# Optimization experiments

Measured on AMD Instinct MI355X. Metric: run time of the kernel, lower is better.

The kernel has to match this reference:

```python
import jax, jax.numpy as jnp
import numpy as np

B, L, D, H, FFN = 4, 1024, 1024, 16, 4096
DPH = D // H
EPS = 1e-5

def layer_norm(x, g, b):
    mu = jnp.mean(x, axis=-1, keepdims=True)
    var = jnp.mean(jnp.square(x - mu), axis=-1, keepdims=True)
    return (x - mu) * jax.lax.rsqrt(var + EPS) * g + b

def setup_inputs() -> dict:
    key = jax.random.key(0)
    ks = jax.random.split(key, 12)
    s = 0.02
    return {
        "inputs": jax.random.normal(ks[0], (B, L, D), dtype=jnp.float32),
        "Wq": jax.random.normal(ks[1], (D, D), dtype=jnp.float32) * s,
        "bq": jnp.zeros((D,), jnp.float32),
        "Wk": jax.random.normal(ks[2], (D, D), dtype=jnp.float32) * s,
        "bk": jnp.zeros((D,), jnp.float32),
        "Wv": jax.random.normal(ks[3], (D, D), dtype=jnp.float32) * s,
        "bv": jnp.zeros((D,), jnp.float32),
        "Wo": jax.random.normal(ks[4], (D, D), dtype=jnp.float32) * s,
        "bo": jnp.zeros((D,), jnp.float32),
        "ln1_g": jnp.ones((D,), jnp.float32),
        "ln1_b": jnp.zeros((D,), jnp.float32),
        "W1": jax.random.normal(ks[5], (D, FFN), dtype=jnp.float32) * s,  # conv1d k=1 == linear
        "b1": jnp.zeros((FFN,), jnp.float32),
        "W2": jax.random.normal(ks[6], (FFN, D), dtype=jnp.float32) * s,
        "b2": jnp.zeros((D,), jnp.float32),
        "ln2_g": jnp.ones((D,), jnp.float32),
        "ln2_b": jnp.zeros((D,), jnp.float32),
    }

def reference(inputs, Wq, bq, Wk, bk, Wv, bv, Wo, bo, ln1_g, ln1_b,
              W1, b1, W2, b2, ln2_g, ln2_b):
    residual = inputs
    # QKV projections, then the original's raw view(B*H, L, DPH) split (NOT a transpose split)
    q = (inputs @ Wq + bq).reshape(B * H, L, DPH)
    k = (inputs @ Wk + bk).reshape(B * H, L, DPH)
    v = (inputs @ Wv + bv).reshape(B * H, L, DPH)
    scale = DPH ** -0.5
    scores = jnp.einsum('bqd,bkd->bqk', q, k) * scale  # [B*H, L, L]
    attention = jax.nn.softmax(scores, axis=-1)
    context = jnp.einsum('bqk,bkd->bqd', attention, v).reshape(B, L, D)
    out = context @ Wo + bo
    out = layer_norm(residual + out, ln1_g, ln1_b)
    # Positionwise FFN: two 1x1 conv1d == two linears with relu
    ffn = jax.nn.relu(out @ W1 + b1) @ W2 + b2
    out = layer_norm(out + ffn, ln2_g, ln2_b)
    return out, attention
```

## Files before the change

kernel.cpp:

```cpp
#include <hip/hip_runtime.h>
#include <hip/hip_bf16.h>
#include <stdint.h>


using bf16_t  = __hip_bfloat16;
using short8  = __attribute__((ext_vector_type(8))) short;
using short4v = __attribute__((ext_vector_type(4))) short;
using f32x4   = __attribute__((ext_vector_type(4))) float;

#define DEV static __device__ __forceinline__

DEV short bfbits(float f) {
  bf16_t h = __float2bfloat16(f);
  union { bf16_t h; short s; } u; u.h = h; return u.s;
}

DEV void gload_lds16(const bf16_t* g, bf16_t* lds) {
  __builtin_amdgcn_global_load_lds(
      (const __attribute__((address_space(1))) void*)g,
      (__attribute__((address_space(3))) void*)lds, 16, 0, 0);
}

__global__ __launch_bounds__(256) void k_f32_to_bf16(const float* __restrict__ in,
                                                     bf16_t* __restrict__ out) {
  size_t i = ((size_t)blockIdx.x * 256 + threadIdx.x) * 4;
  f32x4 x = *(const f32x4*)(in + i);
  short4v o;
  o[0] = bfbits(x[0]); o[1] = bfbits(x[1]); o[2] = bfbits(x[2]); o[3] = bfbits(x[3]);
  *(short4v*)((short*)out + i) = o;
}

__global__ __launch_bounds__(256) void k_transpose_f32_bf16(const float* __restrict__ in,
                                                            bf16_t* __restrict__ out,
                                                            int R, int C) {
  __shared__ float tile[32][33];
  int tx = threadIdx.x & 31, ty = threadIdx.x >> 5;
  int r0 = blockIdx.y * 32, c0 = blockIdx.x * 32;
  #pragma unroll
  for (int i = 0; i < 4; ++i)
    tile[ty + i * 8][tx] = in[(size_t)(r0 + ty + i * 8) * C + c0 + tx];
  __syncthreads();
  #pragma unroll
  for (int i = 0; i < 4; ++i)
    out[(size_t)(c0 + ty + i * 8) * R + r0 + tx] = __float2bfloat16(tile[tx][ty + i * 8]);
}

__global__ __launch_bounds__(256) void k_transpose4_f32_bf16(
    const float* __restrict__ w0, const float* __restrict__ w1,
    const float* __restrict__ w2, const float* __restrict__ w3,
    bf16_t* __restrict__ o0, bf16_t* __restrict__ o1,
    bf16_t* __restrict__ o2, bf16_t* __restrict__ o3) {
  __shared__ float tile[32][33];
  const int zz = blockIdx.z;
  const float* in = zz == 0 ? w0 : zz == 1 ? w1 : zz == 2 ? w2 : w3;
  bf16_t* out = zz == 0 ? o0 : zz == 1 ? o1 : zz == 2 ? o2 : o3;
  int tx = threadIdx.x & 31, ty = threadIdx.x >> 5;
  int r0 = blockIdx.y * 32, c0 = blockIdx.x * 32;
  #pragma unroll
  for (int i = 0; i < 4; ++i)
    tile[ty + i * 8][tx] = in[(size_t)(r0 + ty + i * 8) * 1024 + c0 + tx];
  __syncthreads();
  #pragma unroll
  for (int i = 0; i < 4; ++i)
    out[(size_t)(c0 + ty + i * 8) * 1024 + r0 + tx] = __float2bfloat16(tile[tx][ty + i * 8]);
}

__global__ __launch_bounds__(256) void k_transpose_bf16_b(const bf16_t* __restrict__ in,
                                                          bf16_t* __restrict__ out,
                                                          int R, int C, long sIn, long sOut) {
  __shared__ bf16_t tile[32][33];
  const bf16_t* inz = in + (size_t)blockIdx.z * sIn;
  bf16_t* outz = out + (size_t)blockIdx.z * sOut;
  int tx = threadIdx.x & 31, ty = threadIdx.x >> 5;
  int r0 = blockIdx.y * 32, c0 = blockIdx.x * 32;
  #pragma unroll
  for (int i = 0; i < 4; ++i)
    tile[ty + i * 8][tx] = inz[(size_t)(r0 + ty + i * 8) * C + c0 + tx];
  __syncthreads();
  #pragma unroll
  for (int i = 0; i < 4; ++i)
    outz[(size_t)(c0 + ty + i * 8) * R + r0 + tx] = tile[tx][ty + i * 8];
}

template<int BM, int BN, bool ALPHA, bool BIAS, bool RELU, bool RESID,
         bool OUTF, bool OUTB, bool QKV3>
__global__ __launch_bounds__(256)
void k_gemm_bt(const bf16_t* __restrict__ A, const bf16_t* __restrict__ Bt,
               float* __restrict__ Cf, bf16_t* __restrict__ Cb,
               const float* __restrict__ bias, const float* __restrict__ bias2,
               const float* __restrict__ bias3, const float* __restrict__ resid,
               int Kdim, int lda, int ldb, int ldc, float alpha) {
  constexpr int BK = 32;
  constexpr int WTM = BM / 2, WTN = BN / 2;
  constexpr int MI = WTM / 16, NI = WTN / 16;
  __shared__ __align__(16) bf16_t sA[BM * BK];
  __shared__ __align__(16) bf16_t sB[BN * BK];

  const int tid = threadIdx.x;
  const int lane = tid & 63;
  const int wv = tid >> 6;
  const int wm = wv & 1, wn = wv >> 1;

  const int gx = gridDim.x;
  const int total = gx * gridDim.y;
  const int lin = blockIdx.y * gx + blockIdx.x;
  const int swz = (lin & 7) * (total >> 3) + (lin >> 3);
  const size_t m0 = (size_t)(swz / gx) * BM;
  const size_t n0 = (size_t)(swz % gx) * BN;

  f32x4 acc[MI][NI] = {};

  const int rr = lane >> 2, cc = (lane & 3) * 8;
  const bf16_t* Arow = A + (m0 + rr) * (size_t)lda + cc;
  const bf16_t* Brow = Bt + (n0 + rr) * (size_t)ldb + cc;

  const int fm = wm * WTM + (lane & 15);
  const int fn = wn * WTN + (lane & 15);
  const int fk = (lane >> 4) * 8;

  for (int k0 = 0; k0 < Kdim; k0 += BK) {
    #pragma unroll
    for (int j = 0; j < BM / 64; ++j) {
      int c = j * 4 + wv;
      gload_lds16(Arow + (size_t)c * 16 * lda + k0, sA + c * 512);
    }
    #pragma unroll
    for (int j = 0; j < BN / 64; ++j) {
      int c = j * 4 + wv;
      gload_lds16(Brow + (size_t)c * 16 * ldb + k0, sB + c * 512);
    }
    __syncthreads();

    short8 av[MI], bvv[NI];
    #pragma unroll
    for (int mi = 0; mi < MI; ++mi) av[mi] = *(const short8*)(sA + (fm + mi * 16) * BK + fk);
    #pragma unroll
    for (int ni = 0; ni < NI; ++ni) bvv[ni] = *(const short8*)(sB + (fn + ni * 16) * BK + fk);
    #pragma unroll
    for (int mi = 0; mi < MI; ++mi)
      #pragma unroll
      for (int ni = 0; ni < NI; ++ni)
        acc[mi][ni] = __builtin_amdgcn_mfma_f32_16x16x32_bf16(av[mi], bvv[ni],
                                                              acc[mi][ni], 0, 0, 0);
    __syncthreads();
  }

  const int tz = QKV3 ? (int)(n0 >> 10) : 0;
  const float* bp = BIAS ? (QKV3 ? (tz == 0 ? bias : (tz == 1 ? bias2 : bias3))
                                 : bias) : nullptr;
  bf16_t* cb = QKV3 ? (Cb + (size_t)tz * 4194304) : Cb;
  const float qscale = (QKV3 && tz == 0) ? 0.125f : 1.0f;
  const int col0 = (int)n0 + wn * WTN + (lane & 15);
  const int row0 = (int)m0 + wm * WTM + ((lane >> 4) << 2);
  #pragma unroll
  for (int ni = 0; ni < NI; ++ni) {
    const int col = col0 + ni * 16;
    const int colw = QKV3 ? (col & 1023) : col;
    const float bval = BIAS ? bp[colw] : 0.0f;
    #pragma unroll
    for (int mi = 0; mi < MI; ++mi) {
      #pragma unroll
      for (int r = 0; r < 4; ++r) {
        int row = row0 + mi * 16 + r;
        float v = acc[mi][ni][r];
        if (ALPHA) v *= alpha;
        v += bval;
        if (QKV3) v *= qscale;
        size_t off = (size_t)row * ldc + colw;
        if (RESID) v += resid[off];
        if (RELU) v = fmaxf(v, 0.0f);
        if (OUTF) Cf[off] = v;
        if (OUTB) cb[off] = __float2bfloat16(v);
      }
    }
  }
}

__global__ __launch_bounds__(256) void k_flash_attn(const bf16_t* __restrict__ Qb,
                                                    const bf16_t* __restrict__ Kb,
                                                    const bf16_t* __restrict__ Vt,
                                                    float* __restrict__ attn,
                                                    bf16_t* __restrict__ ctx) {
  constexpr int LP = 72;
  __shared__ __align__(16) bf16_t sQ[128][LP];
  __shared__ __align__(16) bf16_t sK[2][64][LP];
  __shared__ __align__(16) bf16_t sV[2][64][LP];
  __shared__ __align__(16) bf16_t sP[128][LP];

  const int tid = threadIdx.x;
  const int lane = tid & 63;
  const int wv = tid >> 6;
  const int z = blockIdx.y;
  const int m0 = blockIdx.x * 128;

  const bf16_t* Qz = Qb + (size_t)z * 65536;
  const bf16_t* Kz = Kb + (size_t)z * 65536;
  const bf16_t* Vz = Vt + (size_t)z * 65536;
  float* az = attn + (size_t)z * 1048576;
  bf16_t* cz = ctx + (size_t)z * 65536;

  const int sr = tid >> 3, sc = (tid & 7) * 8;

  #pragma unroll
  for (int j = 0; j < 4; ++j)
    *(short8*)(&sQ[j * 32 + sr][sc]) =
        *(const short8*)(Qz + (size_t)(m0 + j * 32 + sr) * 64 + sc);
  __syncthreads();

  const int fr = lane & 15;
  const int fk = (lane >> 4) * 8;
  const int crow = (lane >> 4) << 2;

  short8 qf[2][2];
  #pragma unroll
  for (int mi = 0; mi < 2; ++mi)
    #pragma unroll
    for (int ks = 0; ks < 2; ++ks)
      qf[mi][ks] = *(const short8*)(&sQ[wv * 32 + mi * 16 + fr][ks * 32 + fk]);

  float m_run[2][4], s_run[2][4];
  #pragma unroll
  for (int mi = 0; mi < 2; ++mi)
    #pragma unroll
    for (int r = 0; r < 4; ++r) { m_run[mi][r] = -1e30f; s_run[mi][r] = 0.0f; }

  short8 kreg[2], vreg[2];

  #pragma unroll
  for (int j = 0; j < 2; ++j)
    kreg[j] = *(const short8*)(Kz + (size_t)(j * 32 + sr) * 64 + sc);
  #pragma unroll
  for (int j = 0; j < 2; ++j)
    *(short8*)(&sK[0][j * 32 + sr][sc]) = kreg[j];
  #pragma unroll
  for (int j = 0; j < 2; ++j)
    kreg[j] = *(const short8*)(Kz + (size_t)(64 + j * 32 + sr) * 64 + sc);
  __syncthreads();

  for (int c = 0; c < 16; ++c) {
    const int cur = c & 1;
    if (c + 1 < 16) {
      #pragma unroll
      for (int j = 0; j < 2; ++j)
        *(short8*)(&sK[cur ^ 1][j * 32 + sr][sc]) = kreg[j];
    }
    if (c + 2 < 16) {
      #pragma unroll
      for (int j = 0; j < 2; ++j)
        kreg[j] = *(const short8*)(Kz + (size_t)((c + 2) * 64 + j * 32 + sr) * 64 + sc);
    }
    f32x4 acc[2][4] = {};
    __builtin_amdgcn_s_setprio(1);
    #pragma unroll
    for (int ks = 0; ks < 2; ++ks) {
      short8 bf[4];
      #pragma unroll
      for (int ni = 0; ni < 4; ++ni)
        bf[ni] = *(const short8*)(&sK[cur][ni * 16 + fr][ks * 32 + fk]);
      #pragma unroll
      for (int mi = 0; mi < 2; ++mi)
        #pragma unroll
        for (int ni = 0; ni < 4; ++ni)
          acc[mi][ni] = __builtin_amdgcn_mfma_f32_16x16x32_bf16(qf[mi][ks], bf[ni],
                                                                acc[mi][ni], 0, 0, 0);
    }
    __builtin_amdgcn_s_setprio(0);
    #pragma unroll
    for (int mi = 0; mi < 2; ++mi)
      #pragma unroll
      for (int r = 0; r < 4; ++r) {
        float mx = acc[mi][0][r];
        #pragma unroll
        for (int ni = 1; ni < 4; ++ni) mx = fmaxf(mx, acc[mi][ni][r]);
        #pragma unroll
        for (int o = 1; o < 16; o <<= 1) mx = fmaxf(mx, __shfl_xor(mx, o, 64));
        float mn = fmaxf(m_run[mi][r], mx);
        float se = 0.0f;
        #pragma unroll
        for (int ni = 0; ni < 4; ++ni) se += __expf(acc[mi][ni][r] - mn);
        #pragma unroll
        for (int o = 1; o < 16; o <<= 1) se += __shfl_xor(se, o, 64);
        s_run[mi][r] = s_run[mi][r] * __expf(m_run[mi][r] - mn) + se;
        m_run[mi][r] = mn;
      }
    __syncthreads();
  }

  float inv_s[2][4];
  #pragma unroll
  for (int mi = 0; mi < 2; ++mi)
    #pragma unroll
    for (int r = 0; r < 4; ++r) inv_s[mi][r] = 1.0f / s_run[mi][r];

  #pragma unroll
  for (int j = 0; j < 2; ++j) {
    kreg[j] = *(const short8*)(Kz + (size_t)(j * 32 + sr) * 64 + sc);
    vreg[j] = *(const short8*)(Vz + (size_t)(j * 32 + sr) * 1024 + sc);
  }
  #pragma unroll
  for (int j = 0; j < 2; ++j) {
    *(short8*)(&sK[0][j * 32 + sr][sc]) = kreg[j];
    *(short8*)(&sV[0][j * 32 + sr][sc]) = vreg[j];
  }
  #pragma unroll
  for (int j = 0; j < 2; ++j) {
    kreg[j] = *(const short8*)(Kz + (size_t)(64 + j * 32 + sr) * 64 + sc);
    vreg[j] = *(const short8*)(Vz + (size_t)(j * 32 + sr) * 1024 + 64 + sc);
  }
  __syncthreads();

  f32x4 cacc[2][4] = {};
  for (int c = 0; c < 16; ++c) {
    const int cur = c & 1;
    const int c0 = c * 64;
    if (c + 1 < 16) {
      #pragma unroll
      for (int j = 0; j < 2; ++j) {
        *(short8*)(&sK[cur ^ 1][j * 32 + sr][sc]) = kreg[j];
        *(short8*)(&sV[cur ^ 1][j * 32 + sr][sc]) = vreg[j];
      }
    }
    if (c + 2 < 16) {
      #pragma unroll
      for (int j = 0; j < 2; ++j) {
        kreg[j] = *(const short8*)(Kz + (size_t)((c + 2) * 64 + j * 32 + sr) * 64 + sc);
        vreg[j] = *(const short8*)(Vz + (size_t)(j * 32 + sr) * 1024 + (c + 2) * 64 + sc);
      }
    }
    f32x4 acc[2][4] = {};
    __builtin_amdgcn_s_setprio(1);
    #pragma unroll
    for (int ks = 0; ks < 2; ++ks) {
      short8 bf[4];
      #pragma unroll
      for (int ni = 0; ni < 4; ++ni)
        bf[ni] = *(const short8*)(&sK[cur][ni * 16 + fr][ks * 32 + fk]);
      #pragma unroll
      for (int mi = 0; mi < 2; ++mi)
        #pragma unroll
        for (int ni = 0; ni < 4; ++ni)
          acc[mi][ni] = __builtin_amdgcn_mfma_f32_16x16x32_bf16(qf[mi][ks], bf[ni],
                                                                acc[mi][ni], 0, 0, 0);
    }
    __builtin_amdgcn_s_setprio(0);
    #pragma unroll
    for (int mi = 0; mi < 2; ++mi)
      #pragma unroll
      for (int ni = 0; ni < 4; ++ni)
        #pragma unroll
        for (int r = 0; r < 4; ++r) {
          int row = wv * 32 + mi * 16 + crow + r;
          float p = __expf(acc[mi][ni][r] - m_run[mi][r]) * inv_s[mi][r];
          __builtin_nontemporal_store(p, &az[(size_t)(m0 + row) * 1024 + c0 + ni * 16 + fr]);
          sP[row][ni * 16 + fr] = __float2bfloat16(p);
        }
    asm volatile("s_waitcnt lgkmcnt(0)" ::: "memory");
    __builtin_amdgcn_sched_barrier(0);
    __builtin_amdgcn_s_setprio(1);
    #pragma unroll
    for (int ks = 0; ks < 2; ++ks) {
      short8 pa[2], vb[4];
      #pragma unroll
      for (int mi = 0; mi < 2; ++mi)
        pa[mi] = *(const short8*)(&sP[wv * 32 + mi * 16 + fr][ks * 32 + fk]);
      #pragma unroll
      for (int ni = 0; ni < 4; ++ni)
        vb[ni] = *(const short8*)(&sV[cur][ni * 16 + fr][ks * 32 + fk]);
      #pragma unroll
      for (int mi = 0; mi < 2; ++mi)
        #pragma unroll
        for (int ni = 0; ni < 4; ++ni)
          cacc[mi][ni] = __builtin_amdgcn_mfma_f32_16x16x32_bf16(pa[mi], vb[ni],
                                                                 cacc[mi][ni], 0, 0, 0);
    }
    __builtin_amdgcn_s_setprio(0);
    __syncthreads();
  }

  #pragma unroll
  for (int mi = 0; mi < 2; ++mi)
    #pragma unroll
    for (int ni = 0; ni < 4; ++ni)
      #pragma unroll
      for (int r = 0; r < 4; ++r) {
        int row = wv * 32 + mi * 16 + crow + r;
        cz[(size_t)(m0 + row) * 64 + ni * 16 + fr] = __float2bfloat16(cacc[mi][ni][r]);
      }
}

__global__ __launch_bounds__(256) void k_layernorm(float* __restrict__ io,
                                                   bf16_t* __restrict__ ob,
                                                   const float* __restrict__ g,
                                                   const float* __restrict__ bta) {
  float* r = io + (size_t)blockIdx.x * 1024;
  const int t = threadIdx.x;
  f32x4 x = *(const f32x4*)(r + t * 4);
  float s = x[0] + x[1] + x[2] + x[3];
  float s2 = x[0] * x[0] + x[1] * x[1] + x[2] * x[2] + x[3] * x[3];
  #pragma unroll
  for (int o = 32; o > 0; o >>= 1) { s += __shfl_xor(s, o, 64); s2 += __shfl_xor(s2, o, 64); }
  __shared__ float as[4], as2[4];
  if ((t & 63) == 0) { as[t >> 6] = s; as2[t >> 6] = s2; }
  __syncthreads();
  s = as[0] + as[1] + as[2] + as[3];
  s2 = as2[0] + as2[1] + as2[2] + as2[3];
  float mu = s * (1.0f / 1024.0f);
  float var = s2 * (1.0f / 1024.0f) - mu * mu;
  float rs = rsqrtf(var + 1e-5f);
  f32x4 gg = *(const f32x4*)(g + t * 4);
  f32x4 bb = *(const f32x4*)(bta + t * 4);
  f32x4 y;
  #pragma unroll
  for (int i = 0; i < 4; ++i) y[i] = (x[i] - mu) * rs * gg[i] + bb[i];
  *(f32x4*)(r + t * 4) = y;
  if (ob) {
    short4v o4;
    o4[0] = bfbits(y[0]); o4[1] = bfbits(y[1]); o4[2] = bfbits(y[2]); o4[3] = bfbits(y[3]);
    *(short4v*)((short*)ob + (size_t)blockIdx.x * 1024 + t * 4) = o4;
  }
}

extern "C" void kernel_launch(void* const* d_in, const int* in_sizes, int n_in,
                              void* d_out, int out_size, void* d_ws, size_t ws_size,
                              hipStream_t stream) {
  (void)in_sizes; (void)n_in; (void)out_size;
  const float* inputs = (const float*)d_in[0];
  const float* Wq = (const float*)d_in[1];  const float* bq = (const float*)d_in[2];
  const float* Wk = (const float*)d_in[3];  const float* bk = (const float*)d_in[4];
  const float* Wv = (const float*)d_in[5];  const float* bv = (const float*)d_in[6];
  const float* Wo = (const float*)d_in[7];  const float* bo = (const float*)d_in[8];
  const float* ln1g = (const float*)d_in[9];  const float* ln1b = (const float*)d_in[10];
  const float* W1 = (const float*)d_in[11]; const float* b1 = (const float*)d_in[12];
  const float* W2 = (const float*)d_in[13]; const float* b2 = (const float*)d_in[14];
  const float* ln2g = (const float*)d_in[15]; const float* ln2b = (const float*)d_in[16];

  const size_t MB = 1ull << 20;
  if (ws_size < 96 * MB) return;

  char* ws = (char*)d_ws;
  bf16_t* WQT  = (bf16_t*)(ws + 0 * MB);
  bf16_t* WKT  = (bf16_t*)(ws + 2 * MB);
  bf16_t* WVT  = (bf16_t*)(ws + 4 * MB);
  bf16_t* WOT  = (bf16_t*)(ws + 6 * MB);
  bf16_t* W1T  = (bf16_t*)(ws + 8 * MB);
  bf16_t* W2T  = (bf16_t*)(ws + 16 * MB);
  bf16_t* XB   = (bf16_t*)(ws + 24 * MB);
  bf16_t* QB   = (bf16_t*)(ws + 32 * MB);
  bf16_t* KB   = (bf16_t*)(ws + 40 * MB);
  bf16_t* VB   = (bf16_t*)(ws + 48 * MB);
  bf16_t* VT   = (bf16_t*)(ws + 56 * MB);
  bf16_t* CTX  = (bf16_t*)(ws + 24 * MB);
  float*  OUT1F = (float*)(ws + 40 * MB);
  bf16_t* OUT1B = (bf16_t*)(ws + 32 * MB);
  bf16_t* HB   = (bf16_t*)(ws + 64 * MB);

  float* outF = (float*)d_out;
  float* attn = outF + 4194304;

  k_f32_to_bf16<<<4096, 256, 0, stream>>>(inputs, XB);
  k_transpose4_f32_bf16<<<dim3(32, 32, 4), 256, 0, stream>>>(Wq, Wk, Wv, Wo,
                                                             WQT, WKT, WVT, WOT);
  k_transpose_f32_bf16<<<dim3(128, 32), 256, 0, stream>>>(W1, W1T, 1024, 4096);
  k_transpose_f32_bf16<<<dim3(32, 128), 256, 0, stream>>>(W2, W2T, 4096, 1024);

  k_gemm_bt<128, 128, false, true, false, false, false, true, true>
      <<<dim3(24, 32), 256, 0, stream>>>(XB, WQT, nullptr, QB, bq, bk, bv, nullptr,
                                         1024, 1024, 1024, 1024, 1.0f);

  k_transpose_bf16_b<<<dim3(2, 32, 64), 256, 0, stream>>>(VB, VT, 1024, 64, 65536, 65536);

  k_flash_attn<<<dim3(8, 64), 256, 0, stream>>>(QB, KB, VT, attn, CTX);

  k_gemm_bt<128, 64, false, true, false, true, true, false, false>
      <<<dim3(16, 32), 256, 0, stream>>>(CTX, WOT, OUT1F, nullptr, bo, nullptr, nullptr,
                                         inputs, 1024, 1024, 1024, 1024, 1.0f);

  k_layernorm<<<4096, 256, 0, stream>>>(OUT1F, OUT1B, ln1g, ln1b);

  k_gemm_bt<128, 128, false, true, true, false, false, true, false>
      <<<dim3(32, 32), 256, 0, stream>>>(OUT1B, W1T, nullptr, HB, b1, nullptr, nullptr,
                                         nullptr, 1024, 1024, 1024, 4096, 1.0f);

  k_gemm_bt<128, 64, false, true, false, true, true, false, false>
      <<<dim3(16, 32), 256, 0, stream>>>(HB, W2T, outF, nullptr, b2, nullptr, nullptr,
                                         OUT1F, 4096, 4096, 4096, 1024, 1.0f);

  k_layernorm<<<4096, 256, 0, stream>>>(outF, nullptr, ln2g, ln2b);
}
```

Baseline: 666.4 us.

## Swizzle flash-attention LDS tiles, defer softmax reductions, remap block order

Replaces the padded LDS arrays with unpadded 64-wide tiles using an XOR swizzle on K, V and P to avoid bank conflicts while cutting LDS footprint. It also drops the Q staging in LDS by loading MFMA fragments straight from global memory. The per-chunk cross-lane max/sum shuffles in the first pass become lane-local running stats, merged once with a log-sum-exp combine at the end. Block indices are remapped so neighbouring blocks cover different heads, changing cache locality. Together these aim to reduce shared memory pressure and shuffle overhead.

Result: faster. 645.2 us (-3.2%).

```diff
diff --git a/kernel.cpp b/kernel.cpp
--- a/kernel.cpp
+++ b/kernel.cpp
@@ -181,17 +181,18 @@
                                                     const bf16_t* __restrict__ Vt,
                                                     float* __restrict__ attn,
                                                     bf16_t* __restrict__ ctx) {
-  constexpr int LP = 72;
-  __shared__ __align__(16) bf16_t sQ[128][LP];
-  __shared__ __align__(16) bf16_t sK[2][64][LP];
-  __shared__ __align__(16) bf16_t sV[2][64][LP];
-  __shared__ __align__(16) bf16_t sP[128][LP];
+  __shared__ __align__(16) bf16_t sK[2][64][64];
+  __shared__ __align__(16) bf16_t sV[2][64][64];
+  __shared__ __align__(16) bf16_t sP[128][64];
 
   const int tid = threadIdx.x;
   const int lane = tid & 63;
   const int wv = tid >> 6;
-  const int z = blockIdx.y;
-  const int m0 = blockIdx.x * 128;
+
+  const int lin = blockIdx.y * 8 + blockIdx.x;
+  const int swz = (lin & 7) * 64 + (lin >> 3);
+  const int z = swz >> 3;
+  const int m0 = (swz & 7) * 128;
 
   const bf16_t* Qz = Qb + (size_t)z * 65536;
   const bf16_t* Kz = Kb + (size_t)z * 65536;
@@ -200,29 +201,26 @@
   bf16_t* cz = ctx + (size_t)z * 65536;
 
   const int sr = tid >> 3, sc = (tid & 7) * 8;
-
-  #pragma unroll
-  for (int j = 0; j < 4; ++j)
-    *(short8*)(&sQ[j * 32 + sr][sc]) =
-        *(const short8*)(Qz + (size_t)(m0 + j * 32 + sr) * 64 + sc);
-  __syncthreads();
+  const int scx = sc ^ ((sr & 7) << 3);
 
   const int fr = lane & 15;
   const int fk = (lane >> 4) * 8;
   const int crow = (lane >> 4) << 2;
+  const int rko = (fr & 7) << 3;
 
   short8 qf[2][2];
   #pragma unroll
   for (int mi = 0; mi < 2; ++mi)
     #pragma unroll
     for (int ks = 0; ks < 2; ++ks)
-      qf[mi][ks] = *(const short8*)(&sQ[wv * 32 + mi * 16 + fr][ks * 32 + fk]);
-
-  float m_run[2][4], s_run[2][4];
+      qf[mi][ks] = *(const short8*)(Qz + (size_t)(m0 + wv * 32 + mi * 16 + fr) * 64 +
+                                    ks * 32 + fk);
+
+  float m_ln[2][4], s_ln[2][4];
   #pragma unroll
   for (int mi = 0; mi < 2; ++mi)
     #pragma unroll
-    for (int r = 0; r < 4; ++r) { m_run[mi][r] = -1e30f; s_run[mi][r] = 0.0f; }
+    for (int r = 0; r < 4; ++r) { m_ln[mi][r] = -1e30f; s_ln[mi][r] = 0.0f; }
 
   short8 kreg[2], vreg[2];
 
@@ -231,7 +229,7 @@
     kreg[j] = *(const short8*)(Kz + (size_t)(j * 32 + sr) * 64 + sc);
   #pragma unroll
   for (int j = 0; j < 2; ++j)
-    *(short8*)(&sK[0][j * 32 + sr][sc]) = kreg[j];
+    *(short8*)(&sK[0][j * 32 + sr][scx]) = kreg[j];
   #pragma unroll
   for (int j = 0; j < 2; ++j)
     kreg[j] = *(const short8*)(Kz + (size_t)(64 + j * 32 + sr) * 64 + sc);
@@ -242,7 +240,7 @@
     if (c + 1 < 16) {
       #pragma unroll
       for (int j = 0; j < 2; ++j)
-        *(short8*)(&sK[cur ^ 1][j * 32 + sr][sc]) = kreg[j];
+        *(short8*)(&sK[cur ^ 1][j * 32 + sr][scx]) = kreg[j];
     }
     if (c + 2 < 16) {
       #pragma unroll
@@ -256,7 +254,7 @@
       short8 bf[4];
       #pragma unroll
       for (int ni = 0; ni < 4; ++ni)
-        bf[ni] = *(const short8*)(&sK[cur][ni * 16 + fr][ks * 32 + fk]);
+        bf[ni] = *(const short8*)(&sK[cur][ni * 16 + fr][(ks * 32 + fk) ^ rko]);
       #pragma unroll
       for (int mi = 0; mi < 2; ++mi)
         #pragma unroll
@@ -269,28 +267,36 @@
     for (int mi = 0; mi < 2; ++mi)
       #pragma unroll
       for (int r = 0; r < 4; ++r) {
-        float mx = acc[mi][0][r];
-        #pragma unroll
-        for (int ni = 1; ni < 4; ++ni) mx = fmaxf(mx, acc[mi][ni][r]);
-        #pragma unroll
-        for (int o = 1; o < 16; o <<= 1) mx = fmaxf(mx, __shfl_xor(mx, o, 64));
-        float mn = fmaxf(m_run[mi][r], mx);
+        float cm = fmaxf(fmaxf(acc[mi][0][r], acc[mi][1][r]),
+                         fmaxf(acc[mi][2][r], acc[mi][3][r]));
+        float mo = m_ln[mi][r];
+        float mn = fmaxf(mo, cm);
         float se = 0.0f;
         #pragma unroll
         for (int ni = 0; ni < 4; ++ni) se += __expf(acc[mi][ni][r] - mn);
-        #pragma unroll
-        for (int o = 1; o < 16; o <<= 1) se += __shfl_xor(se, o, 64);
-        s_run[mi][r] = s_run[mi][r] * __expf(m_run[mi][r] - mn) + se;
-        m_run[mi][r] = mn;
+        s_ln[mi][r] = s_ln[mi][r] * __expf(mo - mn) + se;
+        m_ln[mi][r] = mn;
       }
     __syncthreads();
   }
 
-  float inv_s[2][4];
+  float m_run[2][4], inv_s[2][4];
   #pragma unroll
   for (int mi = 0; mi < 2; ++mi)
     #pragma unroll
-    for (int r = 0; r < 4; ++r) inv_s[mi][r] = 1.0f / s_run[mi][r];
+    for (int r = 0; r < 4; ++r) {
+      float m = m_ln[mi][r], s = s_ln[mi][r];
+      #pragma unroll
+      for (int o = 1; o < 16; o <<= 1) {
+        float m2 = __shfl_xor(m, o, 64);
+        float s2 = __shfl_xor(s, o, 64);
+        float mn = fmaxf(m, m2);
+        s = s * __expf(m - mn) + s2 * __expf(m2 - mn);
+        m = mn;
+      }
+      m_run[mi][r] = m;
+      inv_s[mi][r] = 1.0f / s;
+    }
 
   #pragma unroll
   for (int j = 0; j < 2; ++j) {
@@ -299,8 +305,8 @@
   }
   #pragma unroll
   for (int j = 0; j < 2; ++j) {
-    *(short8*)(&sK[0][j * 32 + sr][sc]) = kreg[j];
-    *(short8*)(&sV[0][j * 32 + sr][sc]) = vreg[j];
+    *(short8*)(&sK[0][j * 32 + sr][scx]) = kreg[j];
+    *(short8*)(&sV[0][j * 32 + sr][scx]) = vreg[j];
   }
   #pragma unroll
   for (int j = 0; j < 2; ++j) {
@@ -316,8 +322,8 @@
     if (c + 1 < 16) {
       #pragma unroll
       for (int j = 0; j < 2; ++j) {
-        *(short8*)(&sK[cur ^ 1][j * 32 + sr][sc]) = kreg[j];
-        *(short8*)(&sV[cur ^ 1][j * 32 + sr][sc]) = vreg[j];
+        *(short8*)(&sK[cur ^ 1][j * 32 + sr][scx]) = kreg[j];
+        *(short8*)(&sV[cur ^ 1][j * 32 + sr][scx]) = vreg[j];
       }
     }
     if (c + 2 < 16) {
@@ -334,7 +340,7 @@
       short8 bf[4];
       #pragma unroll
       for (int ni = 0; ni < 4; ++ni)
-        bf[ni] = *(const short8*)(&sK[cur][ni * 16 + fr][ks * 32 + fk]);
+        bf[ni] = *(const short8*)(&sK[cur][ni * 16 + fr][(ks * 32 + fk) ^ rko]);
       #pragma unroll
       for (int mi = 0; mi < 2; ++mi)
         #pragma unroll
@@ -352,7 +358,7 @@
           int row = wv * 32 + mi * 16 + crow + r;
           float p = __expf(acc[mi][ni][r] - m_run[mi][r]) * inv_s[mi][r];
           __builtin_nontemporal_store(p, &az[(size_t)(m0 + row) * 1024 + c0 + ni * 16 + fr]);
-          sP[row][ni * 16 + fr] = __float2bfloat16(p);
+          sP[row][(ni * 16 + fr) ^ (((crow + r) & 7) << 3)] = __float2bfloat16(p);
         }
     asm volatile("s_waitcnt lgkmcnt(0)" ::: "memory");
     __builtin_amdgcn_sched_barrier(0);
@@ -362,10 +368,10 @@
       short8 pa[2], vb[4];
       #pragma unroll
       for (int mi = 0; mi < 2; ++mi)
-        pa[mi] = *(const short8*)(&sP[wv * 32 + mi * 16 + fr][ks * 32 + fk]);
+        pa[mi] = *(const short8*)(&sP[wv * 32 + mi * 16 + fr][(ks * 32 + fk) ^ rko]);
       #pragma unroll
       for (int ni = 0; ni < 4; ++ni)
-        vb[ni] = *(const short8*)(&sV[cur][ni * 16 + fr][ks * 32 + fk]);
+        vb[ni] = *(const short8*)(&sV[cur][ni * 16 + fr][(ks * 32 + fk) ^ rko]);
       #pragma unroll
       for (int mi = 0; mi < 2; ++mi)
         #pragma unroll
```
